# Optimization experiments

Hardware: AMD Instinct MI355X
Metric: run time of the kernel (lower is better)

Reference implementation:

```python
import jax, jax.numpy as jnp
import numpy as np

HEADS = 4  # opt['heads']; attention_dim=128 -> d_k=32


def setup_inputs() -> dict:
    key = jax.random.key(0)
    ks = jax.random.split(key, 8)
    N, E, IN_F, ATT = 50000, 1600000, 256, 128
    x = jax.random.normal(ks[0], (N, IN_F), dtype=jnp.float32)
    edge = jax.random.randint(ks[1], (2, E), 0, N, dtype=jnp.int64)
    Qw = jax.random.normal(ks[2], (ATT, IN_F), dtype=jnp.float32) * 0.02
    Qb = jax.random.normal(ks[3], (ATT,), dtype=jnp.float32) * 0.02
    Kw = jax.random.normal(ks[4], (ATT, IN_F), dtype=jnp.float32) * 0.02
    Kb = jax.random.normal(ks[5], (ATT,), dtype=jnp.float32) * 0.02
    Vw = jax.random.normal(ks[6], (ATT, IN_F), dtype=jnp.float32) * 0.02
    Vb = jax.random.normal(ks[7], (ATT,), dtype=jnp.float32) * 0.02
    return {"x": x, "edge": edge, "Qw": Qw, "Qb": Qb, "Kw": Kw, "Kb": Kb, "Vw": Vw, "Vb": Vb}


def reference(x, edge, Qw, Qb, Kw, Kb, Vw, Vb):
    N = x.shape[0]
    att = Qw.shape[0]
    d_k = att // HEADS
    inv_sqrt_dk = np.float32(1.0 / np.sqrt(d_k))
    # projections, split into heads: [N, h, d_k]
    q = (x @ Qw.T + Qb).reshape(N, HEADS, d_k)
    k = (x @ Kw.T + Kb).reshape(N, HEADS, d_k)
    v = (x @ Vw.T + Vb).reshape(N, HEADS, d_k)
    src, dst = edge[0], edge[1]
    # per-edge dot-product scores over d_k: [E, h]
    scores = jnp.einsum('ehd,ehd->eh', q[src], k[dst]) * inv_sqrt_dk
    # segment softmax grouped by source node (edge[0])
    m = jax.ops.segment_max(scores, src, num_segments=N)  # [N, h]
    ex = jnp.exp(scores - m[src])
    denom = jax.ops.segment_sum(ex, src, num_segments=N)  # [N, h]
    attn = ex / denom[src]  # [E, h]
    # spmm per head: out[src] += attn * v[dst]; fused over heads
    out = jax.ops.segment_sum(attn[:, :, None] * v[dst], src, num_segments=N)  # [N, h, d_k]
    # torch cat over heads == head-major flatten
    return out.reshape(N, att)
```

## Files before the change

### kernel.cpp

```cpp
#include <hip/hip_runtime.h>

#define HEADS 4
#define ATT   128
#define INF   256
#define DK    32
#define KVROW 384
#define BSTRIDE 10240

typedef __attribute__((ext_vector_type(8))) short bf16x8;
typedef __attribute__((ext_vector_type(4))) float f32x4;
typedef __attribute__((ext_vector_type(2))) float f32x2;

__device__ __forceinline__ unsigned short f2bf(float f) {
    unsigned u = __float_as_uint(f);
    unsigned r = u + 0x7fffu + ((u >> 16) & 1u);
    return (unsigned short)(r >> 16);
}

__device__ __forceinline__ unsigned char f2fp8(float f) {
    return (unsigned char)(__builtin_amdgcn_cvt_pk_fp8_f32(f, f, 0, false) & 0xff);
}

__device__ __forceinline__ void gload_lds16(const void* g, void* s) {
    __builtin_amdgcn_global_load_lds(
        (const __attribute__((address_space(1))) void*)g,
        (__attribute__((address_space(3))) void*)s,
        16, 0, 0);
}

__global__ __launch_bounds__(256) void cast3_kernel(const float* __restrict__ a,
                                                    const float* __restrict__ b,
                                                    const float* __restrict__ c,
                                                    unsigned short* __restrict__ out,
                                                    int* __restrict__ gbcnt, int n8) {
    if (blockIdx.x == 0 && blockIdx.y == 0) gbcnt[threadIdx.x] = 0;
    const float* in = (blockIdx.y == 0) ? a : (blockIdx.y == 1) ? b : c;
    unsigned short* o = out + (size_t)blockIdx.y * n8 * 8;
    int stride = gridDim.x * 256;
    for (int i = blockIdx.x * 256 + threadIdx.x; i < n8; i += stride) {
        float4 p = ((const float4*)in)[(size_t)i * 2];
        float4 q = ((const float4*)in)[(size_t)i * 2 + 1];
        uint4 w;
        w.x = (unsigned)f2bf(p.x) | ((unsigned)f2bf(p.y) << 16);
        w.y = (unsigned)f2bf(p.z) | ((unsigned)f2bf(p.w) << 16);
        w.z = (unsigned)f2bf(q.x) | ((unsigned)f2bf(q.y) << 16);
        w.w = (unsigned)f2bf(q.z) | ((unsigned)f2bf(q.w) << 16);
        ((uint4*)o)[i] = w;
    }
}

__global__ __launch_bounds__(256) void proj_mfma(
    const float* __restrict__ x,
    const unsigned short* __restrict__ wb,
    const float* __restrict__ Bq, const float* __restrict__ Bk, const float* __restrict__ Bv,
    unsigned short* __restrict__ qout, unsigned char* __restrict__ kv, int N)
{
    __shared__ unsigned short As[128 * 32];
    __shared__ unsigned short Bs[128 * 32];

    const int t  = threadIdx.x;
    const int l  = t & 63;
    const int w  = t >> 6;
    const int wr = w >> 1, wc = w & 1;
    const int n0 = blockIdx.x * 128;
    const int mat = blockIdx.y;
    const unsigned short* W = wb + (size_t)mat * 128 * 256;

    f32x4 zero = {0.f, 0.f, 0.f, 0.f};
    f32x4 acc[4][4];
#pragma unroll
    for (int m = 0; m < 4; ++m)
#pragma unroll
        for (int n = 0; n < 4; ++n) acc[m][n] = zero;

    for (int k0 = 0; k0 < INF; k0 += 32) {
#pragma unroll
        for (int j = 0; j < 2; ++j) {
            int c = j * 256 + t;
            int row = c >> 2, part = c & 3;
            int gr = n0 + row; if (gr > N - 1) gr = N - 1;
            const float4* xp = (const float4*)&x[(size_t)gr * INF + k0 + part * 8];
            float4 a = xp[0], b = xp[1];
            uint4 o;
            o.x = (unsigned)f2bf(a.x) | ((unsigned)f2bf(a.y) << 16);
            o.y = (unsigned)f2bf(a.z) | ((unsigned)f2bf(a.w) << 16);
            o.z = (unsigned)f2bf(b.x) | ((unsigned)f2bf(b.y) << 16);
            o.w = (unsigned)f2bf(b.z) | ((unsigned)f2bf(b.w) << 16);
            *(uint4*)&As[(size_t)c * 8] = o;
        }
#pragma unroll
        for (int j = 0; j < 2; ++j) {
            int c = j * 256 + t;
            int row = c >> 2, part = c & 3;
            gload_lds16(W + (size_t)row * INF + k0 + part * 8,
                        &Bs[(size_t)(j * 256 + (w << 6)) * 8]);
        }
        __syncthreads();

        bf16x8 af[4], bfr[4];
#pragma unroll
        for (int m = 0; m < 4; ++m) {
            int row = wr * 64 + m * 16 + (l & 15);
            af[m] = *(const bf16x8*)&As[row * 32 + (l >> 4) * 8];
        }
#pragma unroll
        for (int n = 0; n < 4; ++n) {
            int row = wc * 64 + n * 16 + (l & 15);
            bfr[n] = *(const bf16x8*)&Bs[row * 32 + (l >> 4) * 8];
        }
#pragma unroll
        for (int m = 0; m < 4; ++m)
#pragma unroll
            for (int n = 0; n < 4; ++n)
                acc[m][n] = __builtin_amdgcn_mfma_f32_16x16x32_bf16(af[m], bfr[n], acc[m][n], 0, 0, 0);
        __syncthreads();
    }

    const float* bias = (mat == 0) ? Bq : ((mat == 1) ? Bk : Bv);

#pragma unroll
    for (int m = 0; m < 4; ++m) {
#pragma unroll
        for (int r = 0; r < 4; ++r) {
            int node = n0 + wr * 64 + m * 16 + (l >> 4) * 4 + r;
            if (node < N) {
                unsigned char* kvrow = kv + (size_t)node * KVROW;
#pragma unroll
                for (int n = 0; n < 4; ++n) {
                    int col = wc * 64 + n * 16 + (l & 15);
                    float val = acc[m][n][r] + bias[col];
                    if (mat == 0) {
                        qout[(size_t)node * ATT + col] = f2bf(val);
                    } else if (mat == 1) {
                        kvrow[col] = f2fp8(val * 16.0f);
                    } else {
                        *(unsigned short*)(kvrow + 128 + col * 2) = f2bf(val);
                    }
                }
            }
        }
    }
}

#define PCHUNK 4096
__global__ __launch_bounds__(256) void partA_kernel(const int* __restrict__ e32, int E,
                                                    int* __restrict__ gbcnt,
                                                    unsigned* __restrict__ eperm) {
    __shared__ int hist[256];
    __shared__ int lcur[256];
    __shared__ int s_is64;
    const int t = threadIdx.x;
    const int base = blockIdx.x * PCHUNK;

    if (t == 0) s_is64 = 1;
    hist[t] = 0;
    __syncthreads();
    if (e32[2 * t + 1] != 0) s_is64 = 0;
    __syncthreads();
    const int is64 = s_is64;

    int s[16], d[16];
    if (is64) {
#pragma unroll
        for (int j = 0; j < 8; ++j) {
            int e2 = base + j * 512 + 2 * t;
            s[2 * j] = -1; s[2 * j + 1] = -1; d[2 * j] = 0; d[2 * j + 1] = 0;
            if (e2 + 1 < E) {
                uint4 us = *(const uint4*)&e32[(size_t)2 * e2];
                uint4 ud = *(const uint4*)&e32[(size_t)2 * ((size_t)E + e2)];
                s[2 * j] = (int)us.x; d[2 * j] = (int)ud.x;
                s[2 * j + 1] = (int)us.z; d[2 * j + 1] = (int)ud.z;
            } else if (e2 < E) {
                s[2 * j] = e32[(size_t)2 * e2];
                d[2 * j] = e32[(size_t)2 * ((size_t)E + e2)];
            }
        }
    } else {
#pragma unroll
        for (int j = 0; j < 16; ++j) {
            int e = base + j * 256 + t;
            s[j] = -1; d[j] = 0;
            if (e < E) { s[j] = e32[e]; d[j] = e32[(size_t)E + e]; }
        }
    }
#pragma unroll
    for (int j = 0; j < 16; ++j)
        if (s[j] >= 0) atomicAdd(&hist[s[j] >> 8], 1);
    __syncthreads();
    int h = hist[t];
    int boff = 0;
    if (h > 0) boff = atomicAdd(&gbcnt[t], h);
    lcur[t] = t * BSTRIDE + boff;
    __syncthreads();
#pragma unroll
    for (int j = 0; j < 16; ++j) {
        if (s[j] >= 0) {
            int pos = atomicAdd(&lcur[s[j] >> 8], 1);
            eperm[pos] = ((unsigned)(s[j] & 255) << 16) | (unsigned)d[j];
        }
    }
}

__global__ __launch_bounds__(512) void partB_kernel(const unsigned* __restrict__ eperm,
                                                    const int* __restrict__ gbcnt,
                                                    uint2* __restrict__ off2,
                                                    int* __restrict__ sdst, int N) {
    __shared__ int hist[256];
    __shared__ int ws[4];
    __shared__ int lcur[256];
    const int b = blockIdx.x;
    const int t = threadIdx.x;
    const int base = b * BSTRIDE;
    const int cntb = gbcnt[b];

    if (t < 256) hist[t] = 0;
    __syncthreads();
    for (int i = t; i < cntb; i += 512)
        atomicAdd(&hist[eperm[base + i] >> 16], 1);
    __syncthreads();

    if (t < 256) {
        const int lane = t & 63, w = t >> 6;
        int x = hist[t];
        int s = x;
#pragma unroll
        for (int d = 1; d < 64; d <<= 1) { int u = __shfl_up(s, d, 64); if (lane >= d) s += u; }
        if (lane == 63) ws[w] = s;
        __syncthreads();
        int carry = 0;
        for (int i = 0; i < w; ++i) carry += ws[i];
        int exc = carry + s - x;
        int node = (b << 8) + t;
        if (node < N) off2[node] = make_uint2((unsigned)(base + exc), (unsigned)(base + exc + x));
        lcur[t] = base + exc;
    } else {
        __syncthreads();
    }
    __syncthreads();

    for (int i = t; i < cntb; i += 512) {
        unsigned p = eperm[base + i];
        int pos = atomicAdd(&lcur[p >> 16], 1);
        sdst[pos] = (int)(p & 0xffffu);
    }
}

__device__ __forceinline__ void pair_acc(unsigned kb, uint2 vv, bool live,
                                         float q0, float q1, float q2, float q3,
                                         float& o0, float& o1, float& o2, float& o3,
                                         float& den) {
    f32x2 k01 = __builtin_amdgcn_cvt_pk_f32_fp8((int)kb, false);
    f32x2 k23 = __builtin_amdgcn_cvt_pk_f32_fp8((int)kb, true);
    float part = fmaf(q0, k01[0], fmaf(q1, k01[1], fmaf(q2, k23[0], q3 * k23[1])));
    part += __shfl_xor(part, 1, 64);
    part += __shfl_xor(part, 2, 64);
    part += __shfl_xor(part, 4, 64);
    float p = live ? exp2f(part) : 0.f;
    den += p;
    float v0 = __uint_as_float(vv.x << 16);
    float v1 = __uint_as_float(vv.x & 0xffff0000u);
    float v2 = __uint_as_float(vv.y << 16);
    float v3 = __uint_as_float(vv.y & 0xffff0000u);
    o0 = fmaf(p, v0, o0);
    o1 = fmaf(p, v1, o1);
    o2 = fmaf(p, v2, o2);
    o3 = fmaf(p, v3, o3);
}

__global__ __launch_bounds__(256) void attn_kernel(
    const unsigned short* __restrict__ qb, const unsigned char* __restrict__ kv,
    const uint2* __restrict__ off2, const int* __restrict__ sdst,
    float* __restrict__ out, int N)
{
    const int wid = blockIdx.x * 4 + (threadIdx.x >> 6);
    const int l = threadIdx.x & 63;
    if (wid >= N) return;
    const uint2 oo = off2[wid];
    const int e0 = (int)oo.x, e1 = (int)oo.y;
    const int half = l >> 5, sub = l & 31;

    const float sc2 = 0.17677669529663687f * 1.4426950408889634f / 16.0f;
    uint2 qw = *(const uint2*)&qb[(size_t)wid * ATT + sub * 4];
    float q0 = __uint_as_float(qw.x << 16) * sc2;
    float q1 = __uint_as_float(qw.x & 0xffff0000u) * sc2;
    float q2 = __uint_as_float(qw.y << 16) * sc2;
    float q3 = __uint_as_float(qw.y & 0xffff0000u) * sc2;
    float o0 = 0.f, o1 = 0.f, o2 = 0.f, o3 = 0.f, den = 0.f;

    for (int base = e0; base < e1; base += 64) {
        int cnt = e1 - base; if (cnt > 64) cnt = 64;
        int dl = sdst[base + (l < cnt ? l : cnt - 1)];
        int j = 0;
        for (; j + 8 <= cnt; j += 8) {
            int d0 = __shfl(dl, j + half, 64);
            int d1 = __shfl(dl, j + 2 + half, 64);
            int d2 = __shfl(dl, j + 4 + half, 64);
            int d3 = __shfl(dl, j + 6 + half, 64);
            const unsigned char* r0 = kv + (size_t)d0 * KVROW;
            const unsigned char* r1 = kv + (size_t)d1 * KVROW;
            const unsigned char* r2 = kv + (size_t)d2 * KVROW;
            const unsigned char* r3 = kv + (size_t)d3 * KVROW;
            unsigned kb0 = *(const unsigned*)(r0 + sub * 4);
            uint2    vv0 = *(const uint2*)(r0 + 128 + sub * 8);
            unsigned kb1 = *(const unsigned*)(r1 + sub * 4);
            uint2    vv1 = *(const uint2*)(r1 + 128 + sub * 8);
            unsigned kb2 = *(const unsigned*)(r2 + sub * 4);
            uint2    vv2 = *(const uint2*)(r2 + 128 + sub * 8);
            unsigned kb3 = *(const unsigned*)(r3 + sub * 4);
            uint2    vv3 = *(const uint2*)(r3 + 128 + sub * 8);
            pair_acc(kb0, vv0, true, q0, q1, q2, q3, o0, o1, o2, o3, den);
            pair_acc(kb1, vv1, true, q0, q1, q2, q3, o0, o1, o2, o3, den);
            pair_acc(kb2, vv2, true, q0, q1, q2, q3, o0, o1, o2, o3, den);
            pair_acc(kb3, vv3, true, q0, q1, q2, q3, o0, o1, o2, o3, den);
        }
        for (; j + 4 <= cnt; j += 4) {
            int d0 = __shfl(dl, j + half, 64);
            int d1 = __shfl(dl, j + 2 + half, 64);
            const unsigned char* r0 = kv + (size_t)d0 * KVROW;
            const unsigned char* r1 = kv + (size_t)d1 * KVROW;
            unsigned kb0 = *(const unsigned*)(r0 + sub * 4);
            uint2    vv0 = *(const uint2*)(r0 + 128 + sub * 8);
            unsigned kb1 = *(const unsigned*)(r1 + sub * 4);
            uint2    vv1 = *(const uint2*)(r1 + 128 + sub * 8);
            pair_acc(kb0, vv0, true, q0, q1, q2, q3, o0, o1, o2, o3, den);
            pair_acc(kb1, vv1, true, q0, q1, q2, q3, o0, o1, o2, o3, den);
        }
        for (; j < cnt; j += 2) {
            int jj = j + half;
            int da = __shfl(dl, jj, 64);
            const unsigned char* r0 = kv + (size_t)da * KVROW;
            unsigned kb0 = *(const unsigned*)(r0 + sub * 4);
            uint2    vv0 = *(const uint2*)(r0 + 128 + sub * 8);
            pair_acc(kb0, vv0, jj < cnt, q0, q1, q2, q3, o0, o1, o2, o3, den);
        }
    }
    den += __shfl_xor(den, 32, 64);
    o0 += __shfl_xor(o0, 32, 64);
    o1 += __shfl_xor(o1, 32, 64);
    o2 += __shfl_xor(o2, 32, 64);
    o3 += __shfl_xor(o3, 32, 64);
    float r = (den > 0.f) ? 1.0f / den : 0.f;
    if (half == 0)
        *(float4*)&out[(size_t)wid * ATT + sub * 4] =
            make_float4(o0 * r, o1 * r, o2 * r, o3 * r);
}

extern "C" void kernel_launch(void* const* d_in, const int* in_sizes, int n_in,
                              void* d_out, int out_size, void* d_ws, size_t ws_size,
                              hipStream_t stream)
{
    const float* x   = (const float*)d_in[0];
    const int*   e32 = (const int*)d_in[1];
    const float* Wq  = (const float*)d_in[2];
    const float* Bq  = (const float*)d_in[3];
    const float* Wk  = (const float*)d_in[4];
    const float* Bk  = (const float*)d_in[5];
    const float* Wv  = (const float*)d_in[6];
    const float* Bv  = (const float*)d_in[7];
    float* out = (float*)d_out;

    const int N = in_sizes[0] / INF;
    const int E = in_sizes[1] / 2;

    char* ws = (char*)d_ws;
    size_t o = 0;
    auto take = [&](size_t bytes) -> char* {
        char* p = ws + o;
        o = (o + bytes + 255) & ~(size_t)255;
        return p;
    };
    unsigned short* wb = (unsigned short*)take((size_t)3 * ATT * INF * 2);
    unsigned short* qb = (unsigned short*)take((size_t)N * ATT * 2);
    unsigned char*  kv = (unsigned char*)take((size_t)N * KVROW);
    uint2* off2  = (uint2*)take((size_t)N * 8);
    int*   gbcnt = (int*)take(1024);
    unsigned* eperm = (unsigned*)take((size_t)256 * BSTRIDE * 4);
    int*   sdst  = (int*)take((size_t)256 * BSTRIDE * 4);
    (void)ws_size; (void)n_in; (void)out_size;

    const int nb = (N + 255) / 256;

    cast3_kernel<<<dim3(16, 3), 256, 0, stream>>>(Wq, Wk, Wv, wb, gbcnt, (ATT * INF) / 8);

    proj_mfma<<<dim3((N + 127) / 128, 3), 256, 0, stream>>>(x, wb, Bq, Bk, Bv, qb, kv, N);

    partA_kernel<<<(E + PCHUNK - 1) / PCHUNK, 256, 0, stream>>>(e32, E, gbcnt, eperm);
    partB_kernel<<<nb, 512, 0, stream>>>(eperm, gbcnt, off2, sdst, N);

    attn_kernel<<<(N + 3) / 4, 256, 0, stream>>>(qb, kv, off2, sdst, out, N);
}
```

Before: 167.1 us.

## Share x tile across Q/K/V in projection GEMM with 6-wave blocks

The projection kernel now uses 384-thread blocks where each of six waves computes one matrix (Q, K or V) for a 64-column chunk. The grid's y dimension now indexes output column chunks (2) instead of the matrix (3), so each x tile is loaded and converted to bf16 once per chunk rather than once per matrix. This cuts redundant fp32 reads of x and the repeated bf16 conversion. In exchange each block holds more LDS for weights, and the bf16 conversion work is spread unevenly across threads.

```diff
diff --git a/kernel.cpp b/kernel.cpp
--- a/kernel.cpp
+++ b/kernel.cpp
@@ -49,22 +49,22 @@
     }
 }
 
-__global__ __launch_bounds__(256) void proj_mfma(
+__global__ __launch_bounds__(384) void proj_mfma(
     const float* __restrict__ x,
     const unsigned short* __restrict__ wb,
     const float* __restrict__ Bq, const float* __restrict__ Bk, const float* __restrict__ Bv,
     unsigned short* __restrict__ qout, unsigned char* __restrict__ kv, int N)
 {
     __shared__ unsigned short As[128 * 32];
-    __shared__ unsigned short Bs[128 * 32];
-
-    const int t  = threadIdx.x;
-    const int l  = t & 63;
-    const int w  = t >> 6;
-    const int wr = w >> 1, wc = w & 1;
-    const int n0 = blockIdx.x * 128;
-    const int mat = blockIdx.y;
-    const unsigned short* W = wb + (size_t)mat * 128 * 256;
+    __shared__ unsigned short Bs[3 * 64 * 32];
+
+    const int t   = threadIdx.x;
+    const int l   = t & 63;
+    const int w   = t >> 6;
+    const int wr  = (w >= 3) ? 1 : 0;
+    const int mat = w - wr * 3;
+    const int ch  = blockIdx.y;
+    const int n0  = blockIdx.x * 128;
 
     f32x4 zero = {0.f, 0.f, 0.f, 0.f};
     f32x4 acc[4][4];
@@ -76,24 +76,28 @@
     for (int k0 = 0; k0 < INF; k0 += 32) {
 #pragma unroll
         for (int j = 0; j < 2; ++j) {
-            int c = j * 256 + t;
-            int row = c >> 2, part = c & 3;
-            int gr = n0 + row; if (gr > N - 1) gr = N - 1;
-            const float4* xp = (const float4*)&x[(size_t)gr * INF + k0 + part * 8];
-            float4 a = xp[0], b = xp[1];
-            uint4 o;
-            o.x = (unsigned)f2bf(a.x) | ((unsigned)f2bf(a.y) << 16);
-            o.y = (unsigned)f2bf(a.z) | ((unsigned)f2bf(a.w) << 16);
-            o.z = (unsigned)f2bf(b.x) | ((unsigned)f2bf(b.y) << 16);
-            o.w = (unsigned)f2bf(b.z) | ((unsigned)f2bf(b.w) << 16);
-            *(uint4*)&As[(size_t)c * 8] = o;
-        }
-#pragma unroll
-        for (int j = 0; j < 2; ++j) {
-            int c = j * 256 + t;
-            int row = c >> 2, part = c & 3;
-            gload_lds16(W + (size_t)row * INF + k0 + part * 8,
-                        &Bs[(size_t)(j * 256 + (w << 6)) * 8]);
+            int task = j * 384 + t;
+            if (task < 512) {
+                int row = task >> 2, part = task & 3;
+                int gr = n0 + row; if (gr > N - 1) gr = N - 1;
+                const float4* xp = (const float4*)&x[(size_t)gr * INF + k0 + part * 8];
+                float4 a = xp[0], b = xp[1];
+                uint4 o;
+                o.x = (unsigned)f2bf(a.x) | ((unsigned)f2bf(a.y) << 16);
+                o.y = (unsigned)f2bf(a.z) | ((unsigned)f2bf(a.w) << 16);
+                o.z = (unsigned)f2bf(b.x) | ((unsigned)f2bf(b.y) << 16);
+                o.w = (unsigned)f2bf(b.z) | ((unsigned)f2bf(b.w) << 16);
+                *(uint4*)&As[(size_t)task * 8] = o;
+            }
+        }
+#pragma unroll
+        for (int r = 0; r < 2; ++r) {
+            int task = r * 384 + t;
+            int mrow = task >> 2, part = task & 3;
+            int mb = mrow >> 6, colrow = mrow & 63;
+            gload_lds16(wb + (size_t)mb * 128 * 256 + (size_t)(ch * 64 + colrow) * 256
+                           + k0 + part * 8,
+                        &Bs[(size_t)(r * 384 + w * 64) * 8]);
         }
         __syncthreads();
 
@@ -101,12 +105,12 @@
 #pragma unroll
         for (int m = 0; m < 4; ++m) {
             int row = wr * 64 + m * 16 + (l & 15);
-            af[m] = *(const bf16x8*)&As[row * 32 + (l >> 4) * 8];
+            af[m] = *(const bf16x8*)&As[(size_t)row * 32 + (l >> 4) * 8];
         }
 #pragma unroll
         for (int n = 0; n < 4; ++n) {
-            int row = wc * 64 + n * 16 + (l & 15);
-            bfr[n] = *(const bf16x8*)&Bs[row * 32 + (l >> 4) * 8];
+            int colrow = n * 16 + (l & 15);
+            bfr[n] = *(const bf16x8*)&Bs[(size_t)(mat * 64 + colrow) * 32 + (l >> 4) * 8];
         }
 #pragma unroll
         for (int m = 0; m < 4; ++m)
@@ -127,7 +131,7 @@
                 unsigned char* kvrow = kv + (size_t)node * KVROW;
 #pragma unroll
                 for (int n = 0; n < 4; ++n) {
-                    int col = wc * 64 + n * 16 + (l & 15);
+                    int col = ch * 64 + n * 16 + (l & 15);
                     float val = acc[m][n][r] + bias[col];
                     if (mat == 0) {
                         qout[(size_t)node * ATT + col] = f2bf(val);
@@ -382,7 +386,7 @@
 
     cast3_kernel<<<dim3(16, 3), 256, 0, stream>>>(Wq, Wk, Wv, wb, gbcnt, (ATT * INF) / 8);
 
-    proj_mfma<<<dim3((N + 127) / 128, 3), 256, 0, stream>>>(x, wb, Bq, Bk, Bv, qb, kv, N);
+    proj_mfma<<<dim3((N + 127) / 128, 2), 384, 0, stream>>>(x, wb, Bq, Bk, Bv, qb, kv, N);
 
     partA_kernel<<<(E + PCHUNK - 1) / PCHUNK, 256, 0, stream>>>(e32, E, gbcnt, eperm);
     partB_kernel<<<nb, 512, 0, stream>>>(eperm, gbcnt, off2, sdst, N);
```

Result: no change. 170.2 us (+1.8%).
